# Optimization experiments

Hardware: AMD Instinct MI355X
Metric: run time of the kernel (lower is better)

The kernel has to match this reference:

```python
import jax, jax.numpy as jnp
import numpy as np

FIXED_SIZE = (160, 160, 160)

def _reference_grid(grid_size):
    # [d1, d2, d3, 3] float32 grid of voxel indices, as in layer_util.get_reference_grid
    ax = [jnp.arange(d, dtype=jnp.float32) for d in grid_size]
    return jnp.stack(jnp.meshgrid(*ax, indexing="ij"), axis=-1)

def _resample_linear(vol, loc):
    # vol: [B, D1, D2, D3]; loc: [B, f1, f2, f3, 3] (voxel coords in vol space)
    B = vol.shape[0]
    dims = vol.shape[1:4]
    max_f = jnp.asarray([d - 1 for d in dims], dtype=loc.dtype)
    max_i = jnp.asarray([d - 1 for d in dims], dtype=jnp.int32)
    locc = jnp.clip(loc, 0.0, max_f)          # clamp to volume bounds
    lo = jnp.floor(locc)
    w = locc - lo                              # trilinear weights in [0,1]
    i0 = lo.astype(jnp.int32)
    i1 = jnp.minimum(i0 + 1, max_i)
    b = jnp.arange(B).reshape(B, 1, 1, 1)
    x0, y0, z0 = i0[..., 0], i0[..., 1], i0[..., 2]
    x1, y1, z1 = i1[..., 0], i1[..., 1], i1[..., 2]
    wx, wy, wz = w[..., 0], w[..., 1], w[..., 2]
    ux, uy, uz = 1.0 - wx, 1.0 - wy, 1.0 - wz
    g = lambda ix, iy, iz: vol[b, ix, iy, iz]  # 8-neighbor gather
    return (g(x0, y0, z0) * ux * uy * uz +
            g(x0, y0, z1) * ux * uy * wz +
            g(x0, y1, z0) * ux * wy * uz +
            g(x0, y1, z1) * ux * wy * wz +
            g(x1, y0, z0) * wx * uy * uz +
            g(x1, y0, z1) * wx * uy * wz +
            g(x1, y1, z0) * wx * wy * uz +
            g(x1, y1, z1) * wx * wy * wz)

def setup_inputs() -> dict:
    key = jax.random.key(0)
    k1, k2 = jax.random.split(key)
    B = 4
    ddf = jax.random.normal(k1, (B,) + FIXED_SIZE + (3,), dtype=jnp.float32)
    image = jax.random.normal(k2, (B,) + FIXED_SIZE, dtype=jnp.float32)
    return {"ddf": ddf, "image": image}

def reference(ddf, image):
    grid_ref = _reference_grid(FIXED_SIZE)[None]      # [1, f1, f2, f3, 3]
    grid_warped = grid_ref + ddf                      # [B, f1, f2, f3, 3]
    return _resample_linear(image, grid_warped)       # [B, f1, f2, f3]
```

## Files before the change

kernel.cpp:

```cpp
#include <hip/hip_runtime.h>

#define D     160
#define D2    (D * D)
#define D3    (D * D * D)
#define NB    4
#define TL    4
#define ZSL   80
#define ZWIN  88
#define WINX  11
#define RING  18
#define PLANE 1024
#define LDSF  (RING * PLANE)
#define TPB   640
#define TPD   (D / TL)
#define NZS   (D / ZSL)
#define CNT   10
#define NRUN  (TPD / CNT)
#define NGRP  (NB * TPD * NZS)
#define NBLK  (NGRP * NRUN)

typedef float f32x2 __attribute__((ext_vector_type(2)));
typedef int   i32x2 __attribute__((ext_vector_type(2)));

__global__ __launch_bounds__(TPB) void warp_kernel(
    const float* __restrict__ ddf,
    const float* __restrict__ image,
    float* __restrict__ out)
{
    extern __shared__ float buf[];

    const int tid  = threadIdx.x;
    const int w    = tid >> 6;
    const int lane = tid & 63;
    const int row  = tid / 40;
    const int zch  = tid - row * 40;
    const int rx   = row >> 2, ry = row & 3, zbl = zch * 2;

    int g    = blockIdx.x;
    int gx8  = (g & 7) * (NBLK / 8) + (g >> 3);
    int yrun = gx8 & 3;
    int t    = gx8 >> 2;
    int zs   = t & 1; t >>= 1;
    int xi   = t % TPD;
    int b    = t / TPD;

    const int yt0    = yrun * (CNT * TL);
    const int xt     = xi * TL, zl = zs * ZSL;
    const int xwb    = xt - 3,  zwb = zl - 4;
    const int volofs = b * D3;
    const float* vol = image + volofs;

    int pfix[4];
#pragma unroll
    for (int k = 0; k < 4; ++k) {
        int f  = k * 256 + lane * 4;
        int sx = f / ZWIN;
        int zo = f - sx * ZWIN;
        int srcx = min(max(xwb + sx, 0), D - 1);
        int srcz = min(max(zwb + zo, 0), D - 4);
        pfix[k] = volofs + srcx * D2 + srcz;
    }

    int su = (yt0 + 33) % RING;
    int ps = su + 14; if (ps >= RING) ps -= RING;

    int   vb  = volofs + (xt + rx) * D2 + (yt0 + ry) * D + (zl + zbl);
    float ygf = (float)(yt0 + ry);
    const float xgf = (float)(xt + rx);
    const float zgf = (float)(zl + zbl);
    int   ywb = yt0 - 3;

    const f32x2 zero2 = {0.0f, 0.0f};
    const f32x2 one2  = {1.0f, 1.0f};
    const f32x2 max2  = {(float)(D - 1), (float)(D - 1)};

    for (int m = 0;; ++m) {
        int L = w + m * 10;
        if (L >= 56) break;
        int pi = L >> 2, k = L & 3;
        int p  = yt0 - 3 + pi;
        int srcy = min(max(p, 0), D - 1);
        int slot = (p + 36) % RING;
        const float* gp = image + pfix[k] + srcy * D;
        __builtin_amdgcn_global_load_lds(
            (const __attribute__((address_space(1))) void*)gp,
            (__attribute__((address_space(3))) void*)(buf + slot * PLANE + k * 256),
            16, 0, 0);
    }
    f32x2 q0, q1, q2, n0 = {0, 0}, n1 = {0, 0}, n2 = {0, 0};
    {
        const float* p = ddf + (size_t)vb * 3;
        q0 = __builtin_nontemporal_load((const f32x2*)p);
        q1 = __builtin_nontemporal_load((const f32x2*)(p + 2));
        q2 = __builtin_nontemporal_load((const f32x2*)(p + 4));
    }
    asm volatile("s_waitcnt vmcnt(0)" ::: "memory");
    __builtin_amdgcn_sched_barrier(0);
    __builtin_amdgcn_s_barrier();
    __builtin_amdgcn_sched_barrier(0);

#pragma unroll 1
    for (int it = 0; it < CNT; ++it) {
        f32x2 dx = {q0.x, q1.y};
        f32x2 dy = {q0.y, q2.x};
        f32x2 dz = {q1.x, q2.y};
        f32x2 xg2 = {xgf, xgf};
        f32x2 yg2 = {ygf, ygf};
        f32x2 zg2 = {zgf, zgf + 1.0f};

        f32x2 fx2 = __builtin_elementwise_min(
                        __builtin_elementwise_max(xg2 + dx, zero2), max2);
        f32x2 fy2 = __builtin_elementwise_min(
                        __builtin_elementwise_max(yg2 + dy, zero2), max2);
        f32x2 fz2 = __builtin_elementwise_min(
                        __builtin_elementwise_max(zg2 + dz, zero2), max2);

        i32x2 X0 = __builtin_convertvector(fx2, i32x2);
        i32x2 Y0 = __builtin_convertvector(fy2, i32x2);
        i32x2 Z0 = __builtin_convertvector(fz2, i32x2);
        f32x2 wx2 = fx2 - __builtin_convertvector(X0, f32x2);
        f32x2 wy2 = fy2 - __builtin_convertvector(Y0, f32x2);
        f32x2 wz2 = fz2 - __builtin_convertvector(Z0, f32x2);

        int ba[2], bc[2];
        unsigned flags = 0, shb = 0;
        f32x2 fb00[2] = {}, fb01[2] = {}, fb10[2] = {}, fb11[2] = {};
#pragma unroll
        for (int j = 0; j < 2; ++j) {
            int x0 = X0[j], y0 = Y0[j], z0 = Z0[j];
            int sx0 = x0 - xwb, sy0 = y0 - ywb, sz0 = z0 - zwb;
            bool inWin = ((unsigned)sx0 <= 9u) & ((unsigned)sy0 <= 8u) &
                         ((unsigned)sz0 <= 86u);
            flags |= (unsigned)inWin << j;
            int csx = min(max(sx0, 0), 9);
            int csy = min(max(sy0, 0), 8);
            int csz = min(max(sz0, 0), 86);
            int t0 = su + csy; if (t0 >= RING) t0 -= RING;
            int t1 = t0 + 1;   if (t1 >= RING) t1 = 0;
            ba[j] = t0 * PLANE + csx * ZWIN + csz;
            bc[j] = t1 * PLANE + csx * ZWIN + csz;
            if (!inWin) {
                int x1 = min(x0 + 1, D - 1);
                int y1 = min(y0 + 1, D - 1);
                int zc = min(z0, D - 2);
                shb |= (unsigned)(z0 > zc) << j;
                fb00[j] = *(const f32x2*)(vol + x0 * D2 + y0 * D + zc);
                fb01[j] = *(const f32x2*)(vol + x0 * D2 + y1 * D + zc);
                fb10[j] = *(const f32x2*)(vol + x1 * D2 + y0 * D + zc);
                fb11[j] = *(const f32x2*)(vol + x1 * D2 + y1 * D + zc);
            }
        }
        __builtin_amdgcn_sched_barrier(0);

        if (it + 1 < CNT) {
            const float* p = ddf + (size_t)(vb + TL * D) * 3;
            n0 = __builtin_nontemporal_load((const f32x2*)p);
            n1 = __builtin_nontemporal_load((const f32x2*)(p + 2));
            n2 = __builtin_nontemporal_load((const f32x2*)(p + 4));
        }
        const bool staged = (it + 2 < CNT);
        if (staged) {
            int ptop = ywb + 14;
            {
                int pi = w >> 2, k = w & 3;
                int p = ptop + pi;
                int srcy = min(p, D - 1);
                int slot = ps + pi; if (slot >= RING) slot -= RING;
                const float* gp = image + pfix[k] + srcy * D;
                __builtin_amdgcn_global_load_lds(
                    (const __attribute__((address_space(1))) void*)gp,
                    (__attribute__((address_space(3))) void*)(buf + slot * PLANE + k * 256),
                    16, 0, 0);
            }
            if (w < 6) {
                int L = w + 10;
                int pi = L >> 2, k = L & 3;
                int p = ptop + pi;
                int srcy = min(p, D - 1);
                int slot = ps + pi; if (slot >= RING) slot -= RING;
                const float* gp = image + pfix[k] + srcy * D;
                __builtin_amdgcn_global_load_lds(
                    (const __attribute__((address_space(1))) void*)gp,
                    (__attribute__((address_space(3))) void*)(buf + slot * PLANE + k * 256),
                    16, 0, 0);
            }
        }
        __builtin_amdgcn_sched_barrier(0);

        float a0s[2], a1s[2], c0s[2], c1s[2], e0s[2], e1s[2], g0s[2], g1s[2];
#pragma unroll
        for (int j = 0; j < 2; ++j) {
            a0s[j] = buf[ba[j]];          a1s[j] = buf[ba[j] + 1];
            c0s[j] = buf[bc[j]];          c1s[j] = buf[bc[j] + 1];
            e0s[j] = buf[ba[j] + ZWIN];   e1s[j] = buf[ba[j] + ZWIN + 1];
            g0s[j] = buf[bc[j] + ZWIN];   g1s[j] = buf[bc[j] + ZWIN + 1];
            if (!((flags >> j) & 1)) {
                bool sh = (shb >> j) & 1;
                a0s[j] = sh ? fb00[j].y : fb00[j].x;  a1s[j] = fb00[j].y;
                c0s[j] = sh ? fb01[j].y : fb01[j].x;  c1s[j] = fb01[j].y;
                e0s[j] = sh ? fb10[j].y : fb10[j].x;  e1s[j] = fb10[j].y;
                g0s[j] = sh ? fb11[j].y : fb11[j].x;  g1s[j] = fb11[j].y;
            }
        }
        f32x2 A0 = {a0s[0], a0s[1]}, A1 = {a1s[0], a1s[1]};
        f32x2 C0 = {c0s[0], c0s[1]}, C1 = {c1s[0], c1s[1]};
        f32x2 E0 = {e0s[0], e0s[1]}, E1 = {e1s[0], e1s[1]};
        f32x2 G0 = {g0s[0], g0s[1]}, G1 = {g1s[0], g1s[1]};

        f32x2 ux2 = one2 - wx2, uy2 = one2 - wy2, uz2 = one2 - wz2;
        f32x2 r2 = (A0 * uz2 + A1 * wz2) * (ux2 * uy2)
                 + (C0 * uz2 + C1 * wz2) * (ux2 * wy2)
                 + (E0 * uz2 + E1 * wz2) * (wx2 * uy2)
                 + (G0 * uz2 + G1 * wz2) * (wx2 * wy2);
        __builtin_nontemporal_store(r2, (f32x2*)(out + vb));
        __builtin_amdgcn_sched_barrier(0);

        if (staged) {
            if (w < 6) { asm volatile("s_waitcnt vmcnt(6)" ::: "memory"); }
            else       { asm volatile("s_waitcnt vmcnt(5)" ::: "memory"); }
        } else {
            asm volatile("s_waitcnt vmcnt(4)" ::: "memory");
        }
        __builtin_amdgcn_sched_barrier(0);
        __builtin_amdgcn_s_barrier();
        __builtin_amdgcn_sched_barrier(0);

        q0 = n0; q1 = n1; q2 = n2;
        vb += TL * D; ygf += (float)TL; ywb += TL;
        su += TL; if (su >= RING) su -= RING;
        ps += TL; if (ps >= RING) ps -= RING;
    }
}

extern "C" void kernel_launch(void* const* d_in, const int* in_sizes, int n_in,
                              void* d_out, int out_size, void* d_ws, size_t ws_size,
                              hipStream_t stream) {
    const float* ddf   = (const float*)d_in[0];
    const float* image = (const float*)d_in[1];
    float* out = (float*)d_out;

    hipFuncSetAttribute((const void*)warp_kernel,
                        hipFuncAttributeMaxDynamicSharedMemorySize,
                        LDSF * (int)sizeof(float));

    warp_kernel<<<NBLK, TPB, LDSF * sizeof(float), stream>>>(ddf, image, out);
}
```

Baseline: 93.13 us.

## Reshape tiles to 8x4x40 to shrink LDS window and halo

Changes the per-block output tile from 4x4x80 to 8x4x40 in x,y,z, shrinking the staged z-window and widening the x-window. The LDS ring shrinks below 64KB, so the max-dynamic-shared-memory attribute call is removed, and the load schedule is recomputed for three partial chunks per plane. The aim is less redundant halo traffic per output and possibly more resident blocks per CU. The cost is more out-of-window fallback global gathers near the narrower z boundaries.

```diff
diff --git a/kernel.cpp b/kernel.cpp
--- a/kernel.cpp
+++ b/kernel.cpp
@@ -4,19 +4,21 @@
 #define D2    (D * D)
 #define D3    (D * D * D)
 #define NB    4
-#define TL    4
-#define ZSL   80
-#define ZWIN  88
-#define WINX  11
+#define TLX   8
+#define TLY   4
+#define ZSL   40
+#define ZWIN  48
+#define WINX  15
 #define RING  18
-#define PLANE 1024
+#define PLANE 720
 #define LDSF  (RING * PLANE)
 #define TPB   640
-#define TPD   (D / TL)
+#define TPDX  (D / TLX)
+#define TPDY  (D / TLY)
 #define NZS   (D / ZSL)
 #define CNT   10
-#define NRUN  (TPD / CNT)
-#define NGRP  (NB * TPD * NZS)
+#define NRUN  (TPDY / CNT)
+#define NGRP  (NB * TPDX * NZS)
 #define NBLK  (NGRP * NRUN)
 
 typedef float f32x2 __attribute__((ext_vector_type(2)));
@@ -32,27 +34,27 @@
     const int tid  = threadIdx.x;
     const int w    = tid >> 6;
     const int lane = tid & 63;
-    const int row  = tid / 40;
-    const int zch  = tid - row * 40;
+    const int row  = tid / 20;
+    const int zch  = tid - row * 20;
     const int rx   = row >> 2, ry = row & 3, zbl = zch * 2;
 
     int g    = blockIdx.x;
     int gx8  = (g & 7) * (NBLK / 8) + (g >> 3);
     int yrun = gx8 & 3;
     int t    = gx8 >> 2;
-    int zs   = t & 1; t >>= 1;
-    int xi   = t % TPD;
-    int b    = t / TPD;
-
-    const int yt0    = yrun * (CNT * TL);
-    const int xt     = xi * TL, zl = zs * ZSL;
-    const int xwb    = xt - 3,  zwb = zl - 4;
+    int zi   = t & 3; t >>= 2;
+    int xi   = t % TPDX;
+    int b    = t / TPDX;
+
+    const int yt0    = yrun * (CNT * TLY);
+    const int xt     = xi * TLX, zl = zi * ZSL;
+    const int xwb    = xt - 3,   zwb = zl - 4;
     const int volofs = b * D3;
     const float* vol = image + volofs;
 
-    int pfix[4];
-#pragma unroll
-    for (int k = 0; k < 4; ++k) {
+    int pfix[3];
+#pragma unroll
+    for (int k = 0; k < 3; ++k) {
         int f  = k * 256 + lane * 4;
         int sx = f / ZWIN;
         int zo = f - sx * ZWIN;
@@ -76,16 +78,18 @@
 
     for (int m = 0;; ++m) {
         int L = w + m * 10;
-        if (L >= 56) break;
-        int pi = L >> 2, k = L & 3;
+        if (L >= 42) break;
+        int pi = L / 3, k = L - pi * 3;
         int p  = yt0 - 3 + pi;
         int srcy = min(max(p, 0), D - 1);
         int slot = (p + 36) % RING;
-        const float* gp = image + pfix[k] + srcy * D;
-        __builtin_amdgcn_global_load_lds(
-            (const __attribute__((address_space(1))) void*)gp,
-            (__attribute__((address_space(3))) void*)(buf + slot * PLANE + k * 256),
-            16, 0, 0);
+        if (k != 2 || lane < 52) {
+            const float* gp = image + pfix[k] + srcy * D;
+            __builtin_amdgcn_global_load_lds(
+                (const __attribute__((address_space(1))) void*)gp,
+                (__attribute__((address_space(3))) void*)(buf + slot * PLANE + k * 256),
+                16, 0, 0);
+        }
     }
     f32x2 q0, q1, q2, n0 = {0, 0}, n1 = {0, 0}, n2 = {0, 0};
     {
@@ -129,12 +133,12 @@
         for (int j = 0; j < 2; ++j) {
             int x0 = X0[j], y0 = Y0[j], z0 = Z0[j];
             int sx0 = x0 - xwb, sy0 = y0 - ywb, sz0 = z0 - zwb;
-            bool inWin = ((unsigned)sx0 <= 9u) & ((unsigned)sy0 <= 8u) &
-                         ((unsigned)sz0 <= 86u);
+            bool inWin = ((unsigned)sx0 <= 13u) & ((unsigned)sy0 <= 8u) &
+                         ((unsigned)sz0 <= 46u);
             flags |= (unsigned)inWin << j;
-            int csx = min(max(sx0, 0), 9);
+            int csx = min(max(sx0, 0), 13);
             int csy = min(max(sy0, 0), 8);
-            int csz = min(max(sz0, 0), 86);
+            int csz = min(max(sz0, 0), 46);
             int t0 = su + csy; if (t0 >= RING) t0 -= RING;
             int t1 = t0 + 1;   if (t1 >= RING) t1 = 0;
             ba[j] = t0 * PLANE + csx * ZWIN + csz;
@@ -153,7 +157,7 @@
         __builtin_amdgcn_sched_barrier(0);
 
         if (it + 1 < CNT) {
-            const float* p = ddf + (size_t)(vb + TL * D) * 3;
+            const float* p = ddf + (size_t)(vb + TLY * D) * 3;
             n0 = __builtin_nontemporal_load((const f32x2*)p);
             n1 = __builtin_nontemporal_load((const f32x2*)(p + 2));
             n2 = __builtin_nontemporal_load((const f32x2*)(p + 4));
@@ -161,28 +165,22 @@
         const bool staged = (it + 2 < CNT);
         if (staged) {
             int ptop = ywb + 14;
-            {
-                int pi = w >> 2, k = w & 3;
-                int p = ptop + pi;
-                int srcy = min(p, D - 1);
-                int slot = ps + pi; if (slot >= RING) slot -= RING;
-                const float* gp = image + pfix[k] + srcy * D;
-                __builtin_amdgcn_global_load_lds(
-                    (const __attribute__((address_space(1))) void*)gp,
-                    (__attribute__((address_space(3))) void*)(buf + slot * PLANE + k * 256),
-                    16, 0, 0);
-            }
-            if (w < 6) {
-                int L = w + 10;
-                int pi = L >> 2, k = L & 3;
-                int p = ptop + pi;
-                int srcy = min(p, D - 1);
-                int slot = ps + pi; if (slot >= RING) slot -= RING;
-                const float* gp = image + pfix[k] + srcy * D;
-                __builtin_amdgcn_global_load_lds(
-                    (const __attribute__((address_space(1))) void*)gp,
-                    (__attribute__((address_space(3))) void*)(buf + slot * PLANE + k * 256),
-                    16, 0, 0);
+#pragma unroll
+            for (int s = 0; s < 2; ++s) {
+                int L = w + s * 10;
+                if (s == 0 || w < 2) {
+                    int pi = L / 3, k = L - pi * 3;
+                    int p = ptop + pi;
+                    int srcy = min(p, D - 1);
+                    int slot = ps + pi; if (slot >= RING) slot -= RING;
+                    if (k != 2 || lane < 52) {
+                        const float* gp = image + pfix[k] + srcy * D;
+                        __builtin_amdgcn_global_load_lds(
+                            (const __attribute__((address_space(1))) void*)gp,
+                            (__attribute__((address_space(3))) void*)(buf + slot * PLANE + k * 256),
+                            16, 0, 0);
+                    }
+                }
             }
         }
         __builtin_amdgcn_sched_barrier(0);
@@ -216,7 +214,7 @@
         __builtin_amdgcn_sched_barrier(0);
 
         if (staged) {
-            if (w < 6) { asm volatile("s_waitcnt vmcnt(6)" ::: "memory"); }
+            if (w < 2) { asm volatile("s_waitcnt vmcnt(6)" ::: "memory"); }
             else       { asm volatile("s_waitcnt vmcnt(5)" ::: "memory"); }
         } else {
             asm volatile("s_waitcnt vmcnt(4)" ::: "memory");
@@ -226,9 +224,9 @@
         __builtin_amdgcn_sched_barrier(0);
 
         q0 = n0; q1 = n1; q2 = n2;
-        vb += TL * D; ygf += (float)TL; ywb += TL;
-        su += TL; if (su >= RING) su -= RING;
-        ps += TL; if (ps >= RING) ps -= RING;
+        vb += TLY * D; ygf += (float)TLY; ywb += TLY;
+        su += TLY; if (su >= RING) su -= RING;
+        ps += TLY; if (ps >= RING) ps -= RING;
     }
 }
 
@@ -239,9 +237,5 @@
     const float* image = (const float*)d_in[1];
     float* out = (float*)d_out;
 
-    hipFuncSetAttribute((const void*)warp_kernel,
-                        hipFuncAttributeMaxDynamicSharedMemorySize,
-                        LDSF * (int)sizeof(float));
-
     warp_kernel<<<NBLK, TPB, LDSF * sizeof(float), stream>>>(ddf, image, out);
 }
```

Measured after the change: 101.9 us. 1.09x slower.
